# Kernel optimization log

Measured on AMD Instinct MI355X. Metric: run time of the kernel, lower is better.

## Reference

```python
import jax, jax.numpy as jnp
import numpy as np

N_QUBITS = 12
N_LAYERS = 2
DIM = 2 ** N_QUBITS  # 4096
BATCH = 1024


def _apply_gate(state, gate, qubit):
    """Apply a batched 2x2 gate to `qubit`. state: (b, 2^n) c64, gate: (b,2,2) c64.
    Mirrors torch _apply_single_qubit_gate: swap qubit axis to front, bmm, swap back."""
    b = state.shape[0]
    s = state.reshape((b,) + (2,) * N_QUBITS)
    ax = N_QUBITS - qubit  # qubit 0 is the last (least-significant) axis
    s = jnp.swapaxes(s, 1, ax)
    s = s.reshape(b, 2, DIM // 2)
    s = jnp.einsum('bij,bjk->bik', gate, s)
    s = s.reshape((b, 2) + (2,) * (N_QUBITS - 1))
    s = jnp.swapaxes(s, 1, ax)
    return s.reshape(b, DIM)


def _ry_gate(angle):
    """RY(theta) = [[cos(t/2), -sin(t/2)], [sin(t/2), cos(t/2)]]; angle: (b,)."""
    c = jnp.cos(angle / 2)
    s = jnp.sin(angle / 2)
    g = jnp.stack([jnp.stack([c, -s], axis=-1),
                   jnp.stack([s, c], axis=-1)], axis=-2)
    return g.astype(jnp.complex64)


def _apply_cnot(state, control, target):
    """CNOT: flip target amplitudes on the control=1 subspace."""
    b = state.shape[0]
    s = state.reshape((b,) + (2,) * N_QUBITS)
    ca = N_QUBITS - control
    ta = N_QUBITS - target
    s = jnp.moveaxis(s, (ca, ta), (1, 2))
    # control=0 slice unchanged; control=1 slice: swap target 0<->1 (flip)
    s = jnp.concatenate([s[:, :1], jnp.flip(s[:, 1:2], axis=2)], axis=1)
    s = jnp.moveaxis(s, (1, 2), (ca, ta))
    return s.reshape(b, DIM)


def _make_signs():
    # Pauli-Z expectation per qubit = sum_s probs[s] * (1 - 2*bit_q(s)); qubit 0 = LSB
    idx = np.arange(DIM)
    bits = (idx[:, None] >> np.arange(N_QUBITS)[None, :]) & 1
    return jnp.asarray(1.0 - 2.0 * bits, dtype=jnp.float32)  # (DIM, n_qubits)

SIGNS = _make_signs()


def setup_inputs() -> dict:
    key = jax.random.key(0)
    kx, kt = jax.random.split(key)
    x = jax.random.normal(kx, (BATCH, N_QUBITS), dtype=jnp.float32)
    thetas = 0.1 * jax.random.normal(kt, (N_LAYERS, N_QUBITS), dtype=jnp.float32)
    return {"x": x, "thetas": thetas}


def reference(x, thetas):
    b = x.shape[0]
    # |0>^n initial state
    state = jnp.zeros((b, DIM), dtype=jnp.complex64).at[:, 0].set(1.0)
    # angle encoding: RY(x_q) on each qubit
    for q in range(N_QUBITS):
        state = _apply_gate(state, _ry_gate(x[:, q]), q)
    # variational layers: RY(theta) per qubit, then cyclic CNOT ring
    for layer in range(N_LAYERS):
        for q in range(N_QUBITS):
            ang = jnp.broadcast_to(thetas[layer, q], (b,))
            state = _apply_gate(state, _ry_gate(ang), q)
        for q in range(N_QUBITS):
            state = _apply_cnot(state, q, (q + 1) % N_QUBITS)
    # Pauli-Z expectations on all qubits: (b, n_qubits)
    probs = jnp.abs(state) ** 2
    return probs @ SIGNS
```

## Files before the change

kernel.cpp:

```cpp
#include <hip/hip_runtime.h>

#define NQ    12
#define BATCH 1024

typedef float v2 __attribute__((ext_vector_type(2)));

template<int P>
__device__ __forceinline__ void ryp_t(v2 A[16], float t) {
#pragma unroll
    for (int m = 0; m < 16; ++m) {
        if ((m & (1 << P)) == 0) {
            const int j = m | (1 << P);
            const v2 Ai = A[m], Aj = A[j];
            A[m] = Ai - t * Aj;
            A[j] = Aj + t * Ai;
        }
    }
}

__device__ __forceinline__ void ry0_t(v2 A[16], float t) {
    const v2 tv = v2{-t, t};
#pragma unroll
    for (int m = 0; m < 16; ++m) {
        const v2 sw = v2{A[m].y, A[m].x};
        A[m] = A[m] + tv * sw;
    }
}

__device__ __forceinline__ float rdlane(float v, int lane) {
    return __uint_as_float(__builtin_amdgcn_readlane(__float_as_uint(v), lane));
}

__global__ __launch_bounds__(128, 2)
void qc_kernel(const float* __restrict__ x, const float* __restrict__ th,
               float* __restrict__ out) {
    __shared__ float buf1[2 * 64 * 33];
    __shared__ float obuf[12 * 2];

    const int b = blockIdx.x;
    const int w = threadIdx.x >> 6;
    const int l = threadIdx.x & 63;
    const float* xb = x + b * NQ;

    const int q_ = l & 31;
    float ang;
    if (l & 32) ang = (q_ < 12) ? 0.5f * th[NQ + q_] : 0.0f;
    else        { const int m_ = (q_ < 12) ? q_ : 11; ang = 0.5f * (xb[m_] + th[m_]); }
    float sv_, cv_;
    __sincosf(ang, &sv_, &cv_);
    const float tl = __fdividef(sv_, cv_);

    float pt = cv_;
    pt *= __shfl_xor(pt, 1, 64);
    pt *= __shfl_xor(pt, 2, 64);
    pt *= __shfl_xor(pt, 4, 64);
    pt *= __shfl_xor(pt, 8, 64);
    const float C = rdlane(pt, 32);

    float c_[NQ], s_[NQ], t1[NQ];
#pragma unroll
    for (int q = 0; q < NQ; ++q) {
        c_[q] = rdlane(cv_, q);
        s_[q] = rdlane(sv_, q);
        t1[q] = rdlane(tl, 32 + q);
    }

    const int l0=l&1, l1=(l>>1)&1, l2=(l>>2)&1, l3=(l>>3)&1, l4=(l>>4)&1, l5=(l>>5)&1;
    float GL = ((l1^l0) ? s_[6] : c_[6]) * ((l2^l1) ? s_[7] : c_[7]);
    GL *= ((l3^l2) ? s_[8] : c_[8]) * ((l4^l3) ? s_[9] : c_[9]);
    GL *= ((l5^l4) ? s_[10] : c_[10]) * ((w^l5) ? s_[11] : c_[11]);
    GL *= C;
    const float GL0 = GL * (l0 ? s_[5] : c_[5]);
    const float GL1 = GL * (l0 ? c_[5] : s_[5]);

    const float f0_0 = w ? s_[0] : c_[0], f0_1 = w ? c_[0] : s_[0];
    const float f1_0 = w ? s_[1] : c_[1], f1_1 = w ? c_[1] : s_[1];

    v2 A[16];
    A[0] = v2{f0_0 * f1_0, f0_1 * f1_1};
    A[1] = v2{f0_0 * f1_1, f0_1 * f1_0};
#pragma unroll
    for (int k = 2; k < 5; ++k) {
#pragma unroll
        for (int m = 0; m < (1 << (k - 1)); ++m) {
            const int bp = (m >> (k - 2)) & 1;
            A[m | (1 << (k - 1))] = A[m] * (bp ? c_[k] : s_[k]);
            A[m]                  = A[m] * (bp ? s_[k] : c_[k]);
        }
    }
#pragma unroll
    for (int m = 0; m < 16; ++m) A[m] *= (m & 8) ? GL1 : GL0;

    ry0_t(A, t1[0]);
    ryp_t<0>(A, t1[1]);
    ryp_t<1>(A, t1[2]);
    ryp_t<2>(A, t1[3]);
    ryp_t<3>(A, t1[4]);

    {
        float* wp = &buf1[w * 2112 + l * 33];
#pragma unroll
        for (int m = 0; m < 16; ++m) { wp[2*m] = A[m].x; wp[2*m+1] = A[m].y; }
    }
    __syncthreads();
    {
        const float swt = w ? t1[11] : -t1[11];
        const int rbase = (l & 32) * 33 + (l & 31);
        const float* ro = &buf1[w * 2112 + rbase];
        const float* rx = &buf1[(1 - w) * 2112 + rbase];
#pragma unroll
        for (int m = 0; m < 16; ++m) {
            const v2 vo = v2{ro[(2*m) * 33], ro[(2*m+1) * 33]};
            const v2 vx = v2{rx[(2*m) * 33], rx[(2*m+1) * 33]};
            A[m] = vo + swt * vx;
        }
    }

    ry0_t(A, t1[5]);
    ryp_t<0>(A, t1[6]);
    ryp_t<1>(A, t1[7]);
    ryp_t<2>(A, t1[8]);
    ryp_t<3>(A, t1[9]);

    {
        const float tt = l5 ? t1[10] : -t1[10];
#pragma unroll
        for (int m = 0; m < 16; ++m) {
            const v2 p = v2{__shfl_xor(A[m].x, 32, 64), __shfl_xor(A[m].y, 32, 64)};
            A[m] = A[m] + tt * p;
        }
    }

#pragma unroll
    for (int m = 0; m < 16; ++m) A[m] *= A[m];

    float S = 0.f;
#pragma unroll
    for (int m = 0; m < 16; ++m) S += A[m].x + A[m].y;
    float d0[16];
#pragma unroll
    for (int m = 0; m < 16; ++m) d0[m] = A[m].x - A[m].y;
    float P1 = 0.f;
#pragma unroll
    for (int i = 0; i < 16; ++i) P1 += d0[i];
    float d1[8];
#pragma unroll
    for (int i = 0; i < 8; ++i) d1[i] = d0[2*i] - d0[2*i+1];
    float P3 = 0.f;
#pragma unroll
    for (int i = 0; i < 8; ++i) P3 += d1[i];
    float d2[4];
#pragma unroll
    for (int i = 0; i < 4; ++i) d2[i] = d1[2*i] - d1[2*i+1];
    const float P7  = d2[0] + d2[1] + d2[2] + d2[3];
    const float d3a = d2[0] - d2[1], d3b = d2[2] - d2[3];
    const float PF  = d3a + d3b;
    const float PV  = d3a - d3b;

    const int pl5 = __popc(l & 31) & 1;
    float y0 = pl5 ? -P1 : P1;
    float y1 = pl5 ? -P3 : P3;
    float y2 = pl5 ? -P7 : P7;
    float y3 = pl5 ? -PF : PF;
    y0 += __shfl_xor(y0, 1, 64); y1 += __shfl_xor(y1, 1, 64);
    y2 += __shfl_xor(y2, 1, 64); y3 += __shfl_xor(y3, 1, 64);
    y0 += __shfl_xor(y0, 2, 64); y1 += __shfl_xor(y1, 2, 64);
    y2 += __shfl_xor(y2, 2, 64); y3 += __shfl_xor(y3, 2, 64);
    const int g = l & 3;
    float y = (g == 0) ? y0 : (g == 1) ? y1 : (g == 2) ? y2 : y3;
    y += __shfl_xor(y,  4, 64);
    y += __shfl_xor(y,  8, 64);
    y += __shfl_xor(y, 16, 64);
    y += __shfl_xor(y, 32, 64);
    if (l < 4) obuf[(5 + l) * 2 + w] = y;

    float wS = S, wV = PV;
#pragma unroll
    for (int k = 0; k < 6; ++k) {
        float pS = __shfl_xor(wS, 1 << k, 64);
        wS = ((l >> k) & 1) ? (pS - wS) : (wS + pS);
        float pV = __shfl_xor(wV, 1 << k, 64);
        wV = ((l >> k) & 1) ? (pV - wV) : (wV + pV);
    }

    if (l == 3)  obuf[1*2 + w]  = wS;
    if (l == 7)  obuf[2*2 + w]  = wS;
    if (l == 15) obuf[3*2 + w]  = wS;
    if (l == 31) { obuf[4*2 + w] = wS; obuf[9*2 + w] = wV; }
    if (l == 62) obuf[0*2 + w]  = wV;
    if (l == 63) { obuf[10*2 + w] = wV; obuf[11*2 + w] = wV; }
    __syncthreads();

    if (threadIdx.x < NQ) {
        const int q = threadIdx.x;
        const float p0 = obuf[q*2 + 0], p1 = obuf[q*2 + 1];
        out[b * NQ + q] = (q == 0 || q == 11) ? (p0 - p1) : (p0 + p1);
    }
}

extern "C" void kernel_launch(void* const* d_in, const int* in_sizes, int n_in,
                              void* d_out, int out_size, void* d_ws, size_t ws_size,
                              hipStream_t stream) {
    const float* x  = (const float*)d_in[0];
    const float* th = (const float*)d_in[1];
    float* out = (float*)d_out;
    (void)in_sizes; (void)n_in; (void)out_size; (void)d_ws; (void)ws_size;

    qc_kernel<<<BATCH, 128, 0, stream>>>(x, th, out);
}
```

Before: 10.26 us.

## Split state across four waves with eight amplitudes per thread

Changes the thread-to-amplitude mapping so each block of 256 threads (four waves) holds the 4096-amplitude state, with 8 real pairs per thread instead of 16. Two qubits now live on wave bits and are mixed via a 4-way shared-memory exchange using vectorized float4 LDS reads. One extra qubit now uses lane shuffles. The aim is more parallelism and shorter per-thread dependency chains, at the cost of more waves per block, extra LDS traffic and a slightly more involved final reduction across four partials.

```diff
diff --git a/kernel.cpp b/kernel.cpp
--- a/kernel.cpp
+++ b/kernel.cpp
@@ -4,11 +4,12 @@
 #define BATCH 1024
 
 typedef float v2 __attribute__((ext_vector_type(2)));
+typedef float v4 __attribute__((ext_vector_type(4)));
 
 template<int P>
-__device__ __forceinline__ void ryp_t(v2 A[16], float t) {
-#pragma unroll
-    for (int m = 0; m < 16; ++m) {
+__device__ __forceinline__ void ryp_t8(v2 A[8], float t) {
+#pragma unroll
+    for (int m = 0; m < 8; ++m) {
         if ((m & (1 << P)) == 0) {
             const int j = m | (1 << P);
             const v2 Ai = A[m], Aj = A[j];
@@ -18,10 +19,10 @@
     }
 }
 
-__device__ __forceinline__ void ry0_t(v2 A[16], float t) {
+__device__ __forceinline__ void ry0_t8(v2 A[8], float t) {
     const v2 tv = v2{-t, t};
 #pragma unroll
-    for (int m = 0; m < 16; ++m) {
+    for (int m = 0; m < 8; ++m) {
         const v2 sw = v2{A[m].y, A[m].x};
         A[m] = A[m] + tv * sw;
     }
@@ -31,15 +32,16 @@
     return __uint_as_float(__builtin_amdgcn_readlane(__float_as_uint(v), lane));
 }
 
-__global__ __launch_bounds__(128, 2)
+__global__ __launch_bounds__(256, 4)
 void qc_kernel(const float* __restrict__ x, const float* __restrict__ th,
                float* __restrict__ out) {
-    __shared__ float buf1[2 * 64 * 33];
-    __shared__ float obuf[12 * 2];
+    __shared__ float buf1[4 * 16 * 68];
+    __shared__ float obuf[12 * 4];
 
     const int b = blockIdx.x;
     const int w = threadIdx.x >> 6;
     const int l = threadIdx.x & 63;
+    const int w0 = w & 1, w1 = w >> 1;
     const float* xb = x + b * NQ;
 
     const int q_ = l & 31;
@@ -66,21 +68,21 @@
     }
 
     const int l0=l&1, l1=(l>>1)&1, l2=(l>>2)&1, l3=(l>>3)&1, l4=(l>>4)&1, l5=(l>>5)&1;
-    float GL = ((l1^l0) ? s_[6] : c_[6]) * ((l2^l1) ? s_[7] : c_[7]);
-    GL *= ((l3^l2) ? s_[8] : c_[8]) * ((l4^l3) ? s_[9] : c_[9]);
-    GL *= ((l5^l4) ? s_[10] : c_[10]) * ((w^l5) ? s_[11] : c_[11]);
-    GL *= C;
-    const float GL0 = GL * (l0 ? s_[5] : c_[5]);
-    const float GL1 = GL * (l0 ? c_[5] : s_[5]);
-
-    const float f0_0 = w ? s_[0] : c_[0], f0_1 = w ? c_[0] : s_[0];
-    const float f1_0 = w ? s_[1] : c_[1], f1_1 = w ? c_[1] : s_[1];
-
-    v2 A[16];
+    float GL = ((l1^l0) ? s_[5] : c_[5]) * ((l2^l1) ? s_[6] : c_[6]);
+    GL *= ((l3^l2) ? s_[7] : c_[7]) * ((l4^l3) ? s_[8] : c_[8]);
+    GL *= ((l5^l4) ? s_[9] : c_[9]) * ((w0^l5) ? s_[10] : c_[10]);
+    GL *= ((w0^w1) ? s_[11] : c_[11]) * C;
+    const float GL0 = GL * (l0 ? s_[4] : c_[4]);
+    const float GL1 = GL * (l0 ? c_[4] : s_[4]);
+
+    const float f0_0 = w1 ? s_[0] : c_[0], f0_1 = w1 ? c_[0] : s_[0];
+    const float f1_0 = w1 ? s_[1] : c_[1], f1_1 = w1 ? c_[1] : s_[1];
+
+    v2 A[8];
     A[0] = v2{f0_0 * f1_0, f0_1 * f1_1};
     A[1] = v2{f0_0 * f1_1, f0_1 * f1_0};
 #pragma unroll
-    for (int k = 2; k < 5; ++k) {
+    for (int k = 2; k < 4; ++k) {
 #pragma unroll
         for (int m = 0; m < (1 << (k - 1)); ++m) {
             const int bp = (m >> (k - 2)) & 1;
@@ -89,79 +91,89 @@
         }
     }
 #pragma unroll
-    for (int m = 0; m < 16; ++m) A[m] *= (m & 8) ? GL1 : GL0;
-
-    ry0_t(A, t1[0]);
-    ryp_t<0>(A, t1[1]);
-    ryp_t<1>(A, t1[2]);
-    ryp_t<2>(A, t1[3]);
-    ryp_t<3>(A, t1[4]);
-
-    {
-        float* wp = &buf1[w * 2112 + l * 33];
-#pragma unroll
-        for (int m = 0; m < 16; ++m) { wp[2*m] = A[m].x; wp[2*m+1] = A[m].y; }
+    for (int m = 0; m < 8; ++m) A[m] *= (m & 4) ? GL1 : GL0;
+
+    ry0_t8(A, t1[0]);
+    ryp_t8<0>(A, t1[1]);
+    ryp_t8<1>(A, t1[2]);
+    ryp_t8<2>(A, t1[3]);
+
+    {
+        float* wp = &buf1[w * 1088 + l];
+#pragma unroll
+        for (int m = 0; m < 8; ++m) {
+            wp[(2*m)   * 68] = A[m].x;
+            wp[(2*m+1) * 68] = A[m].y;
+        }
     }
     __syncthreads();
-    {
-        const float swt = w ? t1[11] : -t1[11];
-        const int rbase = (l & 32) * 33 + (l & 31);
-        const float* ro = &buf1[w * 2112 + rbase];
-        const float* rx = &buf1[(1 - w) * 2112 + rbase];
-#pragma unroll
-        for (int m = 0; m < 16; ++m) {
-            const v2 vo = v2{ro[(2*m) * 33], ro[(2*m+1) * 33]};
-            const v2 vx = v2{rx[(2*m) * 33], rx[(2*m+1) * 33]};
-            A[m] = vo + swt * vx;
-        }
-    }
-
-    ry0_t(A, t1[5]);
-    ryp_t<0>(A, t1[6]);
-    ryp_t<1>(A, t1[7]);
-    ryp_t<2>(A, t1[8]);
-    ryp_t<3>(A, t1[9]);
-
-    {
-        const float tt = l5 ? t1[10] : -t1[10];
-#pragma unroll
-        for (int m = 0; m < 16; ++m) {
+
+    {
+        const float st0 = w0 ? t1[10] : -t1[10];
+        const float st1 = w1 ? t1[11] : -t1[11];
+        const int rbase = (l & 15) * 68 + (l & 48);
+        const float* r00 = &buf1[ w      * 1088 + rbase];
+        const float* r01 = &buf1[(w ^ 1) * 1088 + rbase];
+        const float* r10 = &buf1[(w ^ 2) * 1088 + rbase];
+        const float* r11 = &buf1[(w ^ 3) * 1088 + rbase];
+#pragma unroll
+        for (int k = 0; k < 4; ++k) {
+            const v4 a  = *reinterpret_cast<const v4*>(r00 + 4*k);
+            const v4 bq = *reinterpret_cast<const v4*>(r01 + 4*k);
+            const v4 cq = *reinterpret_cast<const v4*>(r10 + 4*k);
+            const v4 dq = *reinterpret_cast<const v4*>(r11 + 4*k);
+            const v4 u = a  + st0 * bq;
+            const v4 v = cq + st0 * dq;
+            const v4 r = u + st1 * v;
+            A[2*k]   = v2{r.x, r.y};
+            A[2*k+1] = v2{r.z, r.w};
+        }
+    }
+
+    ry0_t8(A, t1[4]);
+    ryp_t8<0>(A, t1[5]);
+    ryp_t8<1>(A, t1[6]);
+    ryp_t8<2>(A, t1[7]);
+
+    {
+        const float tt = (l & 16) ? t1[8] : -t1[8];
+#pragma unroll
+        for (int m = 0; m < 8; ++m) {
+            const v2 p = v2{__shfl_xor(A[m].x, 16, 64), __shfl_xor(A[m].y, 16, 64)};
+            A[m] = A[m] + tt * p;
+        }
+    }
+    {
+        const float tt = (l & 32) ? t1[9] : -t1[9];
+#pragma unroll
+        for (int m = 0; m < 8; ++m) {
             const v2 p = v2{__shfl_xor(A[m].x, 32, 64), __shfl_xor(A[m].y, 32, 64)};
             A[m] = A[m] + tt * p;
         }
     }
 
 #pragma unroll
-    for (int m = 0; m < 16; ++m) A[m] *= A[m];
-
-    float S = 0.f;
-#pragma unroll
-    for (int m = 0; m < 16; ++m) S += A[m].x + A[m].y;
-    float d0[16];
-#pragma unroll
-    for (int m = 0; m < 16; ++m) d0[m] = A[m].x - A[m].y;
-    float P1 = 0.f;
-#pragma unroll
-    for (int i = 0; i < 16; ++i) P1 += d0[i];
-    float d1[8];
-#pragma unroll
-    for (int i = 0; i < 8; ++i) d1[i] = d0[2*i] - d0[2*i+1];
-    float P3 = 0.f;
-#pragma unroll
-    for (int i = 0; i < 8; ++i) P3 += d1[i];
-    float d2[4];
-#pragma unroll
-    for (int i = 0; i < 4; ++i) d2[i] = d1[2*i] - d1[2*i+1];
-    const float P7  = d2[0] + d2[1] + d2[2] + d2[3];
-    const float d3a = d2[0] - d2[1], d3b = d2[2] - d2[3];
-    const float PF  = d3a + d3b;
-    const float PV  = d3a - d3b;
-
-    const int pl5 = __popc(l & 31) & 1;
-    float y0 = pl5 ? -P1 : P1;
-    float y1 = pl5 ? -P3 : P3;
-    float y2 = pl5 ? -P7 : P7;
-    float y3 = pl5 ? -PF : PF;
+    for (int m = 0; m < 8; ++m) A[m] *= A[m];
+
+    float S = 0.f, d0[8];
+#pragma unroll
+    for (int m = 0; m < 8; ++m) { S += A[m].x + A[m].y; d0[m] = A[m].x - A[m].y; }
+    float V1 = 0.f;
+#pragma unroll
+    for (int i = 0; i < 8; ++i) V1 += d0[i];
+    float d1[4];
+#pragma unroll
+    for (int i = 0; i < 4; ++i) d1[i] = d0[2*i] - d0[2*i+1];
+    const float V2 = d1[0] + d1[1] + d1[2] + d1[3];
+    const float d2a = d1[0] - d1[1], d2b = d1[2] - d1[3];
+    const float V3 = d2a + d2b;
+    const float V4 = d2a - d2b;
+
+    const int pl = __popc(l & 15) & 1;
+    float y0 = pl ? -V1 : V1;
+    float y1 = pl ? -V2 : V2;
+    float y2 = pl ? -V3 : V3;
+    float y3 = pl ? -V4 : V4;
     y0 += __shfl_xor(y0, 1, 64); y1 += __shfl_xor(y1, 1, 64);
     y2 += __shfl_xor(y2, 1, 64); y3 += __shfl_xor(y3, 1, 64);
     y0 += __shfl_xor(y0, 2, 64); y1 += __shfl_xor(y1, 2, 64);
@@ -172,9 +184,9 @@
     y += __shfl_xor(y,  8, 64);
     y += __shfl_xor(y, 16, 64);
     y += __shfl_xor(y, 32, 64);
-    if (l < 4) obuf[(5 + l) * 2 + w] = y;
-
-    float wS = S, wV = PV;
+    if (l < 4) obuf[(4 + l) * 4 + w] = y;
+
+    float wS = S, wV = V4;
 #pragma unroll
     for (int k = 0; k < 6; ++k) {
         float pS = __shfl_xor(wS, 1 << k, 64);
@@ -183,18 +195,24 @@
         wV = ((l >> k) & 1) ? (pV - wV) : (wV + pV);
     }
 
-    if (l == 3)  obuf[1*2 + w]  = wS;
-    if (l == 7)  obuf[2*2 + w]  = wS;
-    if (l == 15) obuf[3*2 + w]  = wS;
-    if (l == 31) { obuf[4*2 + w] = wS; obuf[9*2 + w] = wV; }
-    if (l == 62) obuf[0*2 + w]  = wV;
-    if (l == 63) { obuf[10*2 + w] = wV; obuf[11*2 + w] = wV; }
+    if (l == 3)  obuf[1 * 4 + w] = wS;
+    if (l == 7)  obuf[2 * 4 + w] = wS;
+    if (l == 15) obuf[3 * 4 + w] = wS;
+    if (l == 31) obuf[8 * 4 + w] = wV;
+    if (l == 62) obuf[0 * 4 + w] = wV;
+    if (l == 63) obuf[9 * 4 + w] = wV;
     __syncthreads();
 
     if (threadIdx.x < NQ) {
         const int q = threadIdx.x;
-        const float p0 = obuf[q*2 + 0], p1 = obuf[q*2 + 1];
-        out[b * NQ + q] = (q == 0 || q == 11) ? (p0 - p1) : (p0 + p1);
+        const int src = (q >= 10) ? 9 : q;
+        const float p0 = obuf[src * 4 + 0], p1 = obuf[src * 4 + 1];
+        const float p2 = obuf[src * 4 + 2], p3 = obuf[src * 4 + 3];
+        float r;
+        if (q == 0 || q == 11) r = p0 - p1 - p2 + p3;
+        else if (q == 10)      r = p0 - p1 + p2 - p3;
+        else                   r = p0 + p1 + p2 + p3;
+        out[b * NQ + q] = r;
     }
 }
 
@@ -206,5 +224,5 @@
     float* out = (float*)d_out;
     (void)in_sizes; (void)n_in; (void)out_size; (void)d_ws; (void)ws_size;
 
-    qc_kernel<<<BATCH, 128, 0, stream>>>(x, th, out);
-}
+    qc_kernel<<<BATCH, 256, 0, stream>>>(x, th, out);
+}
```

After: 11.55 us. +12.5%, slower.

## Transpose shared-memory exchange layout and fold the lane-32 gate into LDS reads

Applied to the files above, without the earlier changes.

Reshapes the shared-memory buffer so each thread writes its amplitudes down a padded column and reads them back as 128-bit vectors. The read stage now fetches four quadrants (own and partner wave, own and flipped lane-32 half) and applies both the qubit-10 and qubit-11 mixing during the transpose. This removes the 32 cross-lane shuffles that applied the qubit-10 rotation later, at the cost of twice as many LDS reads. It relies on the two rotations commuting with the qubit 5-9 rotations applied in between.

```diff
diff --git a/kernel.cpp b/kernel.cpp
--- a/kernel.cpp
+++ b/kernel.cpp
@@ -4,6 +4,7 @@
 #define BATCH 1024
 
 typedef float v2 __attribute__((ext_vector_type(2)));
+typedef float v4 __attribute__((ext_vector_type(4)));
 
 template<int P>
 __device__ __forceinline__ void ryp_t(v2 A[16], float t) {
@@ -34,7 +35,7 @@
 __global__ __launch_bounds__(128, 2)
 void qc_kernel(const float* __restrict__ x, const float* __restrict__ th,
                float* __restrict__ out) {
-    __shared__ float buf1[2 * 64 * 33];
+    __shared__ __attribute__((aligned(16))) float buf1[2 * 32 * 68];
     __shared__ float obuf[12 * 2];
 
     const int b = blockIdx.x;
@@ -98,21 +99,36 @@
     ryp_t<3>(A, t1[4]);
 
     {
-        float* wp = &buf1[w * 2112 + l * 33];
-#pragma unroll
-        for (int m = 0; m < 16; ++m) { wp[2*m] = A[m].x; wp[2*m+1] = A[m].y; }
+        float* wp = &buf1[w * 2176 + l];
+#pragma unroll
+        for (int m = 0; m < 16; ++m) {
+            wp[(2*m)   * 68] = A[m].x;
+            wp[(2*m+1) * 68] = A[m].y;
+        }
     }
     __syncthreads();
+
     {
-        const float swt = w ? t1[11] : -t1[11];
-        const int rbase = (l & 32) * 33 + (l & 31);
-        const float* ro = &buf1[w * 2112 + rbase];
-        const float* rx = &buf1[(1 - w) * 2112 + rbase];
-#pragma unroll
-        for (int m = 0; m < 16; ++m) {
-            const v2 vo = v2{ro[(2*m) * 33], ro[(2*m+1) * 33]};
-            const v2 vx = v2{rx[(2*m) * 33], rx[(2*m+1) * 33]};
-            A[m] = vo + swt * vx;
+        const float s10 = (l & 32) ? t1[10] : -t1[10];
+        const float s11 = w ? t1[11] : -t1[11];
+        const int basec = (l & 31) * 68;
+        const int ro = (l & 32);
+        const int rf = ro ^ 32;
+        const float* p00 = &buf1[ w      * 2176 + basec + ro];
+        const float* p01 = &buf1[ w      * 2176 + basec + rf];
+        const float* p10 = &buf1[(w ^ 1) * 2176 + basec + ro];
+        const float* p11 = &buf1[(w ^ 1) * 2176 + basec + rf];
+#pragma unroll
+        for (int k = 0; k < 8; ++k) {
+            const v4 a  = *reinterpret_cast<const v4*>(p00 + 4*k);
+            const v4 bq = *reinterpret_cast<const v4*>(p01 + 4*k);
+            const v4 cq = *reinterpret_cast<const v4*>(p10 + 4*k);
+            const v4 dq = *reinterpret_cast<const v4*>(p11 + 4*k);
+            const v4 u = a  + s10 * bq;
+            const v4 v = cq + s10 * dq;
+            const v4 r = u + s11 * v;
+            A[2*k]   = v2{r.x, r.y};
+            A[2*k+1] = v2{r.z, r.w};
         }
     }
 
@@ -121,15 +137,6 @@
     ryp_t<1>(A, t1[7]);
     ryp_t<2>(A, t1[8]);
     ryp_t<3>(A, t1[9]);
-
-    {
-        const float tt = l5 ? t1[10] : -t1[10];
-#pragma unroll
-        for (int m = 0; m < 16; ++m) {
-            const v2 p = v2{__shfl_xor(A[m].x, 32, 64), __shfl_xor(A[m].y, 32, 64)};
-            A[m] = A[m] + tt * p;
-        }
-    }
 
 #pragma unroll
     for (int m = 0; m < 16; ++m) A[m] *= A[m];
```

New measurement: 9.870 us. 3.8% less time.
